# Kernel optimization log

Hardware: AMD Instinct MI355X
Metric: run time of the kernel (lower is better)

Reference implementation:

```python
import jax, jax.numpy as jnp
import numpy as np
import math

H = 12          # num_attention_heads
DH = 64         # attention_head_size
D = H * DH      # hidden_size = 768
LN_EPS = 1e-5
GAUSS_W = 0.3989422804014327
WIDS = [None, 0.1, 1.0, 5.0]


def gauss_weight(L, wid):
    # faithful to generate_gauss_weight: row-normalized Gaussian bump per query pos
    center = (jnp.arange(L, dtype=jnp.float32) / L)[:, None]       # (L,1)
    pos = jnp.linspace(0.0, 1.0, L, dtype=jnp.float32)[None, :]    # (1,L)
    width = max(wid, 0.01) / 9.0                                   # static python scalar
    g = (GAUSS_W / width) * jnp.exp(-(pos - center) ** 2 / (2.0 * width * width))
    return g / jnp.max(g, axis=-1, keepdims=True)                  # (L,L)


def layer_norm(x, g, b):
    mu = jnp.mean(x, axis=-1, keepdims=True)
    var = jnp.mean((x - mu) ** 2, axis=-1, keepdims=True)
    return (x - mu) * jax.lax.rsqrt(var + LN_EPS) * g + b


def bert_attention(x, mask, qkv_w, qkv_b, out_w, out_b, ln_g, ln_b, wid):
    # x: (N,L,D); mask: (N,L,L); qkv_w: (3,D,D); qkv_b: (3,D)
    N, L, _ = x.shape

    def heads(t):  # (N,L,D) -> (N,H,L,DH)
        return t.reshape(N, L, H, DH).transpose(0, 2, 1, 3)

    q = heads(x @ qkv_w[0] + qkv_b[0])
    k = heads(x @ qkv_w[1] + qkv_b[1])
    v = heads(x @ qkv_w[2] + qkv_b[2])

    scores = jnp.einsum('nhqd,nhkd->nhqk', q, k) / math.sqrt(DH)   # (N,H,L,L)
    if wid is not None:
        scores = scores * gauss_weight(L, wid)[None, None]          # multiplicative GMM mask
    scores = scores + (1.0 - mask[:, None, :, :]) * -10000.0
    probs = jax.nn.softmax(scores, axis=-1)                         # dropout = identity (eval)
    ctx = jnp.einsum('nhqk,nhkd->nhqd', probs, v)                   # (N,H,L,DH)
    ctx = ctx.transpose(0, 2, 1, 3).reshape(N, L, D)

    proj = ctx @ out_w + out_b
    return layer_norm(proj + x, ln_g, ln_b)


def setup_inputs() -> dict:
    key = jax.random.key(0)
    ks = jax.random.split(key, 4)
    N, L = 4, 1024
    s = 0.02
    return {
        'input_tensor': jax.random.normal(ks[0], (N, L, D), dtype=jnp.float32),
        'attention_mask': jnp.ones((N, L, L), dtype=jnp.float32),
        'qkv_w': jax.random.normal(ks[1], (4, 3, D, D), dtype=jnp.float32) * s,
        'qkv_b': jnp.zeros((4, 3, D), dtype=jnp.float32),
        'out_w': jax.random.normal(ks[2], (4, D, D), dtype=jnp.float32) * s,
        'out_b': jnp.zeros((4, D), dtype=jnp.float32),
        'ln_g': jnp.ones((4, D), dtype=jnp.float32),
        'ln_b': jnp.zeros((4, D), dtype=jnp.float32),
    }


def reference(input_tensor, attention_mask, qkv_w, qkv_b, out_w, out_b, ln_g, ln_b):
    # pure_block=False path: 4 parallel GMM-masked attention branches, averaged
    outs = [
        bert_attention(input_tensor, attention_mask,
                       qkv_w[i], qkv_b[i], out_w[i], out_b[i], ln_g[i], ln_b[i], WIDS[i])
        for i in range(4)
    ]
    return jnp.mean(jnp.stack(outs, axis=-1), axis=-1)
```

## Files before the change

kernel.cpp:

```cpp
#include <hip/hip_runtime.h>
#include <hip/hip_bf16.h>

#define NB 4
#define LQ 1024
#define NH 12
#define DHD 64
#define DM 768
#define MTOT (NB*LQ)
#define L2E 1.4426950408889634f
#define SMB 11.541560327111708f
#define CFAR 3.3546262790251185e-4f

typedef __attribute__((ext_vector_type(4))) float f32x4;
typedef __attribute__((ext_vector_type(8))) short bf16x8;
typedef __attribute__((ext_vector_type(4))) short short4v;
typedef unsigned short u16;

#if __has_builtin(__builtin_amdgcn_exp2f)
#define EXP2(x) __builtin_amdgcn_exp2f(x)
#else
#define EXP2(x) __expf((x) * 0.6931471805599453f)
#endif

#define VMCNT(n) asm volatile("s_waitcnt vmcnt(" #n ")" ::: "memory")
#define RAW_BAR() __builtin_amdgcn_s_barrier()

__device__ __forceinline__ u16 f2bf(float f){
  union { float f; unsigned int i; } v; v.f = f;
  unsigned int r = v.i + 0x7FFFu + ((v.i >> 16) & 1u);
  return (u16)(r >> 16);
}
__device__ __forceinline__ float bf2f(u16 u){
  union { unsigned int i; float f; } v; v.i = ((unsigned int)u) << 16;
  return v.f;
}
__device__ __forceinline__ unsigned cvt_pk_bf16(float lo, float hi){
  unsigned r;
  asm("v_cvt_pk_bf16_f32 %0, %1, %2" : "=v"(r) : "v"(lo), "v"(hi));
  return r;
}

typedef const __attribute__((address_space(1))) void* gas_t;
typedef __attribute__((address_space(3))) void* las_t;
__device__ __forceinline__ void gload16(const void* g, void* l){
  __builtin_amdgcn_global_load_lds((gas_t)g, (las_t)l, 16, 0, 0);
}

__global__ void k_cvt_x(const float* __restrict__ x, u16* __restrict__ xb){
  int i = (blockIdx.x * 256 + threadIdx.x) * 4;
  float4 v = *reinterpret_cast<const float4*>(x + i);
  short4v o;
  o[0] = (short)f2bf(v.x); o[1] = (short)f2bf(v.y);
  o[2] = (short)f2bf(v.z); o[3] = (short)f2bf(v.w);
  *reinterpret_cast<short4v*>(xb + i) = o;
}

__global__ void k_wt(const float* __restrict__ qkv_w, const float* __restrict__ out_w,
                     u16* __restrict__ wt){
  int mat = blockIdx.z;
  const float* W = (mat < 12) ? (qkv_w + (size_t)mat*DM*DM)
                              : (out_w + (size_t)(mat-12)*DM*DM);
  __shared__ float tile[32][33];
  int j0 = blockIdx.x*32, k0 = blockIdx.y*32;
  int tx = threadIdx.x, ty = threadIdx.y;
  #pragma unroll
  for (int i=0;i<4;i++)
    tile[ty + i*8][tx] = W[(size_t)(k0 + ty + i*8)*DM + j0 + tx];
  __syncthreads();
  u16* dst = wt + (size_t)mat*DM*DM;
  int tid = ty*32 + tx;
  int jj = tid >> 3, kq = tid & 7;
  short4v pk;
  #pragma unroll
  for (int t=0;t<4;t++) pk[t] = (short)f2bf(tile[kq*4 + t][jj]);
  *reinterpret_cast<short4v*>(&dst[(size_t)(j0 + jj)*DM + k0 + kq*4]) = pk;
}

__global__ void k_maskchk(const float* __restrict__ mask, unsigned* __restrict__ flags){
  int qt = blockIdx.x, kt = blockIdx.y, n = blockIdx.z;
  const float* M = mask + ((size_t)(n*LQ) + qt*64)*LQ + kt*64;
  int tid = threadIdx.x;
  int r = tid >> 2, c4 = (tid & 3) * 16;
  int ok = 1;
  #pragma unroll
  for (int j=0;j<4;j++){
    float4 v = *reinterpret_cast<const float4*>(M + (size_t)r*LQ + c4 + j*4);
    ok &= (v.x==1.f) & (v.y==1.f) & (v.z==1.f) & (v.w==1.f);
  }
  __shared__ int sok[4];
  unsigned long long bal = __ballot(ok);
  if ((tid & 63) == 0) sok[tid>>6] = (bal == 0xFFFFFFFFFFFFFFFFull) ? 1 : 0;
  __syncthreads();
  if (tid == 0) flags[((size_t)n*16 + qt)*16 + kt] = sok[0] & sok[1] & sok[2] & sok[3];
}

__global__ __launch_bounds__(256) void k_vsum(const u16* __restrict__ qkvws, float* __restrict__ ps){
  const int nh = blockIdx.x;
  const int b  = blockIdx.y;
  const size_t blk = (size_t)NB*NH*LQ*DHD;
  const u16* Vt = qkvws + (size_t)(b*3+2)*blk + (size_t)nh*DHD*LQ;
  const int tid = threadIdx.x;
  const int dh = tid >> 2, c = tid & 3;
  float* psb = ps + ((size_t)(b*48 + nh)*17)*64;
  float acc = 0.f;
  for (int kt = 0; kt < 16; ++kt){
    if (c == 0) psb[kt*64 + dh] = acc;
    bf16x8 v0 = *reinterpret_cast<const bf16x8*>(&Vt[(size_t)dh*LQ + kt*64 + c*16]);
    bf16x8 v1 = *reinterpret_cast<const bf16x8*>(&Vt[(size_t)dh*LQ + kt*64 + c*16 + 8]);
    float s = 0.f;
    #pragma unroll
    for (int j=0;j<8;j++) s += bf2f((u16)v0[j]) + bf2f((u16)v1[j]);
    s += __shfl_xor(s, 1);
    s += __shfl_xor(s, 2);
    acc += s;
  }
  if (c == 0) psb[16*64 + dh] = acc;
}

__device__ __forceinline__ void gemm_tile32(const u16* __restrict__ Ag,
                                            const u16* __restrict__ Bg,
                                            u16* smem, f32x4 acc[4][4])
{
  const int tid = threadIdx.x, lane = tid & 63, w = tid >> 6;
  const int wr = (w >> 1) * 64, wc = (w & 1) * 64;
  const int rl = lane & 15, q4 = lane >> 4;
  const int srow = tid >> 2;
  const int su = (tid & 3) ^ ((srow >> 1) & 3);

  #define QSTG(buf, k0_) { \
    _Pragma("unroll") \
    for (int r = 0; r < 2; ++r){ \
      gload16(Ag + (size_t)(r*64 + srow)*DM + (k0_) + su*8, smem + (buf)*8192 + r*2048 + tid*8); \
      gload16(Bg + (size_t)(r*64 + srow)*DM + (k0_) + su*8, smem + (buf)*8192 + 4096 + r*2048 + tid*8); \
    } }

  QSTG(0, 0);
  for (int it = 0; it < 24; ++it){
    const int cur = it & 1;
    if (it + 1 < 24){
      QSTG(cur^1, (it+1)*32);
      VMCNT(4);
    } else {
      VMCNT(0);
    }
    RAW_BAR();
    __builtin_amdgcn_sched_barrier(0);
    const u16* al = smem + cur*8192;
    const u16* bl = al + 4096;
    bf16x8 af[4], bfr[4];
    #pragma unroll
    for (int f = 0; f < 4; ++f){
      int ra = wr + f*16 + rl, rb = wc + f*16 + rl;
      int ua = q4 ^ ((ra >> 1) & 3), ub = q4 ^ ((rb >> 1) & 3);
      af[f]  = *reinterpret_cast<const bf16x8*>(&al[ra*32 + ua*8]);
      bfr[f] = *reinterpret_cast<const bf16x8*>(&bl[rb*32 + ub*8]);
    }
    #pragma unroll
    for (int mf=0; mf<4; ++mf)
      #pragma unroll
      for (int nf=0; nf<4; ++nf)
        acc[mf][nf] = __builtin_amdgcn_mfma_f32_16x16x32_bf16(af[mf], bfr[nf], acc[mf][nf], 0,0,0);
    RAW_BAR();
  }
  #undef QSTG
}

__global__ __launch_bounds__(256) void k_qkv(const u16* __restrict__ xb, const u16* __restrict__ wt,
                     const float* __restrict__ qkv_b, u16* __restrict__ qkvws)
{
  __shared__ __align__(16) u16 smem[17408];
  const int bid = blockIdx.x;
  const int orig = (bid & 7) * 288 + (bid >> 3);
  const int m0 = (orig & 31) * 128;
  const int j0 = ((orig >> 5) % 6) * 128;
  const int mat = orig / 192;
  const int t = mat % 3;
  f32x4 acc[4][4] = {};
  gemm_tile32(xb + (size_t)m0*DM, wt + (size_t)mat*DM*DM + (size_t)j0*DM, smem, acc);

  const int tid = threadIdx.x, lane = tid & 63, w = tid >> 6;
  const int wr = (w >> 1) * 64, wc = (w & 1) * 64;
  const int rl = lane & 15, rg = (lane >> 4) * 4;
  const float sc = (t == 0) ? 0.125f : 1.0f;
  const size_t matbase = (size_t)mat * ((size_t)NB*NH*LQ*DHD);
  if (t < 2){
    #pragma unroll
    for (int nf=0; nf<4; ++nf){
      int jc = wc + nf*16 + rl;
      float bias = qkv_b[mat*DM + j0 + jc];
      #pragma unroll
      for (int mf=0; mf<4; ++mf){
        int row = wr + mf*16 + rg;
        #pragma unroll
        for (int i=0;i<4;i++)
          smem[(row+i)*136 + jc] = f2bf((acc[mf][nf][i] + bias) * sc);
      }
    }
    __syncthreads();
    const int n = m0 >> 10, l0 = m0 & 1023;
    const int hbase = j0 >> 6;
    #pragma unroll
    for (int jj=0; jj<8; ++jj){
      int idx = tid + 256*jj;
      int l = idx >> 4, ch = idx & 15;
      bf16x8 v = *reinterpret_cast<const bf16x8*>(&smem[l*136 + ch*8]);
      int hh = hbase + (ch >> 3);
      int dh0 = (ch & 7) * 8;
      *reinterpret_cast<bf16x8*>(
        &qkvws[matbase + ((size_t)(n*NH + hh)*LQ + l0 + l)*DHD + dh0]) = v;
    }
  } else {
    #pragma unroll
    for (int nf=0; nf<4; ++nf){
      int j = j0 + wc + nf*16 + rl;
      float bias = qkv_b[mat*DM + j];
      int h = j >> 6, dh = j & 63;
      #pragma unroll
      for (int mf=0; mf<4; ++mf){
        int mB = m0 + wr + mf*16 + rg;
        int n = mB >> 10, l = mB & 1023;
        short4v pk;
        #pragma unroll
        for (int i=0;i<4;i++) pk[i] = (short)f2bf(acc[mf][nf][i] + bias);
        *reinterpret_cast<short4v*>(&qkvws[matbase + ((size_t)(n*NH + h)*DHD + dh)*LQ + l]) = pk;
      }
    }
  }
}

__global__ __launch_bounds__(512) void k_attn(const u16* __restrict__ qkvws, const float* __restrict__ mask,
                      const unsigned* __restrict__ flags, const float* __restrict__ ps,
                      u16* __restrict__ ctx, float c2_1, float c2_2, float c2_3)
{
  __shared__ __align__(16) u16 kv_lds[2][2][64*64];
  __shared__ __align__(16) u16 p_lds[128*64];
  const int bid = blockIdx.x;
  const int orig = (bid & 7) * 192 + (bid >> 3);
  const int qp = orig & 7;
  const int b  = (orig >> 3) & 3;
  const int nh = orig >> 5;
  const int n = nh / NH, h = nh % NH;
  const float c2 = (b==1) ? c2_1 : (b==2) ? c2_2 : c2_3;
  const bool useG = (b != 0);
  const int tid = threadIdx.x, lane = tid & 63, w = tid >> 6;
  const int wl = w & 3, half = w >> 2;
  const int qt = qp*2 + half;
  const int rl = lane & 15, q4 = lane >> 4, kc8 = q4*8, rg = q4*4;
  const int q0 = qt*64 + wl*16;

  const size_t hb = (size_t)(n*NH + h);
  const size_t blk = (size_t)NB*NH*LQ*DHD;
  const u16* Qb = qkvws + (size_t)(b*3+0)*blk + hb*LQ*DHD;
  const u16* Kb = qkvws + (size_t)(b*3+1)*blk + hb*LQ*DHD;
  const u16* Vt = qkvws + (size_t)(b*3+2)*blk + hb*DHD*LQ;
  const float* Mb = mask + (size_t)n*LQ*LQ;

  bf16x8 qf0 = *reinterpret_cast<const bf16x8*>(&Qb[(size_t)(q0+rl)*DHD + kc8]);
  bf16x8 qf1 = *reinterpret_cast<const bf16x8*>(&Qb[(size_t)(q0+rl)*DHD + 32 + kc8]);

  float srun[4] = {0.f,0.f,0.f,0.f};
  float dmin2[4], cq[4];
  f32x4 o[4] = {};
  #pragma unroll
  for (int i=0;i<4;i++){
    int q = q0 + rg + i;
    float c = (float)q * (1.0f/1024.0f);
    float ksf = floorf(c * 1023.0f + 0.5f);
    float dm = ksf * (1.0f/1023.0f) - c;
    cq[i] = c; dmin2[i] = dm*dm;
  }

  int lo_a, hi_a, lo_b, hi_b, ra_a, ra_b;
  {
    int qa = qp*2, qb = qp*2+1;
    int r0 = 1, r1 = 1;
    for (int t = 0; t < 16; ++t){
      r0 &= (flags[((size_t)n*16 + qa)*16 + t] != 0u) ? 1 : 0;
      r1 &= (flags[((size_t)n*16 + qb)*16 + t] != 0u) ? 1 : 0;
    }
    ra_a = r0; ra_b = r1;
    lo_a = 0; hi_a = 16; lo_b = 0; hi_b = 16;
    if (r0){
      if (b == 1){ lo_a = qa>0?qa-1:0; hi_a = qa<15?qa+2:16; }
      else if (b == 2){ lo_a = qa>5?qa-5:0; hi_a = qa<10?qa+6:16; }
    }
    if (r1){
      if (b == 1){ lo_b = qb>0?qb-1:0; hi_b = qb<15?qb+2:16; }
      else if (b == 2){ lo_b = qb>5?qb-5:0; hi_b = qb<10?qb+6:16; }
    }
  }
  const int mylo = half ? lo_b : lo_a;
  const int myhi = half ? hi_b : hi_a;
  const int myrowall = half ? ra_b : ra_a;
  const int blo = lo_a < lo_b ? lo_a : lo_b;
  const int bhi = hi_a > hi_b ? hi_a : hi_b;
  const int mynt = myhi - mylo;

  if (myrowall && mynt < 16){
    const float* psb = ps + ((size_t)(b*48 + nh)*17)*64;
    #pragma unroll
    for (int nf=0; nf<4; ++nf){
      int dh = nf*16 + rl;
      float sfar = psb[16*64 + dh] - psb[myhi*64 + dh] + psb[mylo*64 + dh];
      float fv = CFAR * sfar;
      #pragma unroll
      for (int i=0;i<4;i++) o[nf][i] = fv;
    }
    float sinit = CFAR * (float)(64*(16 - mynt));
    #pragma unroll
    for (int i=0;i<4;i++) srun[i] = sinit;
  }

  const int r8 = tid >> 3;
  const int uu = (tid & 7) ^ (r8 & 7);

  #define STAGE8(buf, kt_) { \
    gload16(Kb + (size_t)((kt_)*64 + r8)*DHD + uu*8, (u16*)kv_lds[buf][0] + tid*8); \
    gload16(Vt + (size_t)r8*LQ + (kt_)*64 + uu*8, (u16*)kv_lds[buf][1] + tid*8); }

  STAGE8(0, blo);

  const int nloop = bhi - blo;
  for (int it = 0; it < nloop; ++it){
    const int kt = blo + it;
    const int cur = it & 1;
    if (it + 1 < nloop){
      STAGE8(cur^1, kt+1);
      VMCNT(2);
    } else {
      VMCNT(0);
    }
    RAW_BAR();
    __builtin_amdgcn_sched_barrier(0);

    if (kt >= mylo && kt < myhi){
      const bool allones = myrowall || (flags[((size_t)n*16 + qt)*16 + kt] != 0u);
      const u16* kbuf = (const u16*)kv_lds[cur][0];
      const u16* vbuf = (const u16*)kv_lds[cur][1];

      f32x4 sf[4] = {};
      #pragma unroll
      for (int nf=0; nf<4; ++nf){
        int row = nf*16 + rl, sw = (row & 7) << 3;
        bf16x8 kf0 = *reinterpret_cast<const bf16x8*>(&kbuf[row*64 + (kc8 ^ sw)]);
        bf16x8 kf1 = *reinterpret_cast<const bf16x8*>(&kbuf[row*64 + ((32 + kc8) ^ sw)]);
        sf[nf] = __builtin_amdgcn_mfma_f32_16x16x32_bf16(qf0, kf0, sf[nf], 0,0,0);
        sf[nf] = __builtin_amdgcn_mfma_f32_16x16x32_bf16(qf1, kf1, sf[nf], 0,0,0);
      }

      float pv[4][4];
      #pragma unroll
      for (int nf=0; nf<4; ++nf){
        int key = kt*64 + nf*16 + rl;
        float pos = (float)key * (1.0f/1023.0f);
        #pragma unroll
        for (int i=0;i<4;i++){
          float s = sf[nf][i];
          if (useG){
            float d = pos - cq[i];
            float tg = fmaf(-d, d, dmin2[i]);
            s *= EXP2(tg * c2);
          }
          if (!allones){
            int q = q0 + rg + i;
            s = fmaf(1.0f - Mb[(size_t)q*LQ + key], -10000.0f, s);
          }
          float p = EXP2(fmaf(s, L2E, -SMB));
          srun[i] += p;
          pv[nf][i] = p;
        }
      }

      #pragma unroll
      for (int np=0; np<2; ++np)
        #pragma unroll
        for (int i=0;i<4;i++){
          unsigned u = cvt_pk_bf16(pv[np*2][i], pv[np*2+1][i]);
          int row = w*16 + rg + i, sw = (row & 7) << 3;
          p_lds[row*64 + ((np*32 + rl) ^ sw)]      = (u16)(u & 0xffffu);
          p_lds[row*64 + ((np*32 + 16 + rl) ^ sw)] = (u16)(u >> 16);
        }
      asm volatile("s_waitcnt lgkmcnt(0)" ::: "memory");
      __builtin_amdgcn_sched_barrier(0);

      {
        int prow = w*16 + rl, psw = (prow & 7) << 3;
        bf16x8 pa0 = *reinterpret_cast<const bf16x8*>(&p_lds[prow*64 + (kc8 ^ psw)]);
        bf16x8 pa1 = *reinterpret_cast<const bf16x8*>(&p_lds[prow*64 + ((32 + kc8) ^ psw)]);
        #pragma unroll
        for (int nf=0; nf<4; ++nf){
          int row = nf*16 + rl, sw = (row & 7) << 3;
          bf16x8 vv0 = *reinterpret_cast<const bf16x8*>(&vbuf[row*64 + (kc8 ^ sw)]);
          bf16x8 vv1 = *reinterpret_cast<const bf16x8*>(&vbuf[row*64 + ((32 + kc8) ^ sw)]);
          o[nf] = __builtin_amdgcn_mfma_f32_16x16x32_bf16(pa0, vv0, o[nf], 0,0,0);
          o[nf] = __builtin_amdgcn_mfma_f32_16x16x32_bf16(pa1, vv1, o[nf], 0,0,0);
        }
      }
    }
    RAW_BAR();
  }

  #pragma unroll
  for (int off=1; off<16; off<<=1){
    #pragma unroll
    for (int i=0;i<4;i++) srun[i] += __shfl_xor(srun[i], off);
  }
  #pragma unroll
  for (int i=0;i<4;i++){
    float inv = 1.0f / (srun[i] + 1e-35f);
    int q = q0 + rg + i;
    size_t mrow = ((size_t)(n*LQ + q)) * DM;
    #pragma unroll
    for (int nf=0; nf<4; ++nf){
      int d = h*DHD + nf*16 + rl;
      ctx[(size_t)b*((size_t)MTOT*DM) + mrow + d] = f2bf(o[nf][i] * inv);
    }
  }
  #undef STAGE8
}

__global__ __launch_bounds__(256) void k_proj(const u16* __restrict__ ctx, const u16* __restrict__ wt,
                      const float* __restrict__ out_b, u16* __restrict__ proj)
{
  __shared__ __align__(16) u16 smem[17408];
  const int bid = blockIdx.x;
  const int orig = (bid & 7) * 96 + (bid >> 3);
  const int m0 = (orig & 31) * 128;
  const int j0 = ((orig >> 5) % 6) * 128;
  const int b = orig / 192;
  f32x4 acc[4][4] = {};
  gemm_tile32(ctx + (size_t)b*MTOT*DM + (size_t)m0*DM,
              wt + (size_t)(12+b)*DM*DM + (size_t)j0*DM, smem, acc);
  const int tid = threadIdx.x, lane = tid & 63, w = tid >> 6;
  const int wr = (w >> 1) * 64, wc = (w & 1) * 64;
  const int rl = lane & 15, rg = (lane >> 4) * 4;
  #pragma unroll
  for (int nf=0; nf<4; ++nf){
    int jc = wc + nf*16 + rl;
    float bias = out_b[b*DM + j0 + jc];
    #pragma unroll
    for (int mf=0; mf<4; ++mf){
      int row = wr + mf*16 + rg;
      #pragma unroll
      for (int i=0;i<4;i++)
        smem[(row+i)*136 + jc] = f2bf(acc[mf][nf][i] + bias);
    }
  }
  __syncthreads();
  #pragma unroll
  for (int jj=0; jj<8; ++jj){
    int idx = tid + 256*jj;
    int l = idx >> 4, ch = idx & 15;
    bf16x8 v = *reinterpret_cast<const bf16x8*>(&smem[l*136 + ch*8]);
    *reinterpret_cast<bf16x8*>(&proj[((size_t)b*MTOT + m0 + l)*DM + j0 + ch*8]) = v;
  }
}

__global__ __launch_bounds__(256) void k_ln(const float* __restrict__ x, const u16* __restrict__ proj,
                    const float* __restrict__ ln_g, const float* __restrict__ ln_b,
                    float* __restrict__ out)
{
  const int m = blockIdx.x;
  const int tid = threadIdx.x, lane = tid & 63, w = tid >> 6;
  __shared__ float rb[4][2][4];
  float xr[3], acc[3] = {0.f,0.f,0.f};
  #pragma unroll
  for (int c=0;c<3;c++) xr[c] = x[(size_t)m*DM + tid + c*256];
  float vv[4][3], s1[4], s2[4];
  #pragma unroll
  for (int b=0;b<4;b++){
    s1[b] = 0.f; s2[b] = 0.f;
    #pragma unroll
    for (int c=0;c<3;c++){
      float v = bf2f(proj[((size_t)b*MTOT + m)*DM + tid + c*256]) + xr[c];
      vv[b][c] = v; s1[b] += v; s2[b] += v*v;
    }
  }
  #pragma unroll
  for (int b=0;b<4;b++){
    #pragma unroll
    for (int off=32; off>=1; off>>=1){
      s1[b] += __shfl_xor(s1[b], off);
      s2[b] += __shfl_xor(s2[b], off);
    }
    if (lane == 0){ rb[b][0][w] = s1[b]; rb[b][1][w] = s2[b]; }
  }
  __syncthreads();
  #pragma unroll
  for (int b=0;b<4;b++){
    float S1 = rb[b][0][0]+rb[b][0][1]+rb[b][0][2]+rb[b][0][3];
    float S2 = rb[b][1][0]+rb[b][1][1]+rb[b][1][2]+rb[b][1][3];
    float mu = S1 * (1.0f/768.0f);
    float var = S2 * (1.0f/768.0f) - mu*mu;
    float rs = rsqrtf(var + 1e-5f);
    #pragma unroll
    for (int c=0;c<3;c++){
      int j = tid + c*256;
      acc[c] += 0.25f * ((vv[b][c]-mu)*rs*ln_g[b*DM+j] + ln_b[b*DM+j]);
    }
  }
  #pragma unroll
  for (int c=0;c<3;c++) out[(size_t)m*DM + tid + c*256] = acc[c];
}

extern "C" void kernel_launch(void* const* d_in, const int* in_sizes, int n_in,
                              void* d_out, int out_size, void* d_ws, size_t ws_size,
                              hipStream_t stream)
{
  const float* x     = (const float*)d_in[0];
  const float* mask  = (const float*)d_in[1];
  const float* qkv_w = (const float*)d_in[2];
  const float* qkv_b = (const float*)d_in[3];
  const float* out_w = (const float*)d_in[4];
  const float* out_b = (const float*)d_in[5];
  const float* ln_g  = (const float*)d_in[6];
  const float* ln_b  = (const float*)d_in[7];
  float* out = (float*)d_out;
  char* ws = (char*)d_ws;

  u16* xb        = (u16*)(ws);
  unsigned* flags= (unsigned*)(ws);
  float* ps      = (float*)(ws + 8192);
  u16* wt        = (u16*)(ws + 6291456);
  u16* qkv       = (u16*)(ws + 25165824);
  u16* ctx       = (u16*)(ws + 100663296);
  u16* proj      = (u16*)(ws + 25165824);

  float c2[3];
  const float wid[3] = {0.1f, 1.0f, 5.0f};
  for (int i=0;i<3;i++){
    float wdt = wid[i]/9.0f;
    c2[i] = (1.0f/(2.0f*wdt*wdt)) * L2E;
  }

  k_cvt_x<<<dim3(3072), dim3(256), 0, stream>>>(x, xb);
  k_wt<<<dim3(24,24,16), dim3(32,8), 0, stream>>>(qkv_w, out_w, wt);
  k_qkv<<<dim3(2304), dim3(256), 0, stream>>>(xb, wt, qkv_b, qkv);
  k_vsum<<<dim3(48,4), dim3(256), 0, stream>>>(qkv, ps);
  k_maskchk<<<dim3(16,16,4), dim3(256), 0, stream>>>(mask, flags);
  k_attn<<<dim3(1536), dim3(512), 0, stream>>>(qkv, mask, flags, ps, ctx, c2[0], c2[1], c2[2]);
  k_proj<<<dim3(768), dim3(256), 0, stream>>>(ctx, wt, out_b, proj);
  k_ln<<<dim3(4096), dim3(256), 0, stream>>>(x, proj, ln_g, ln_b, out);
}
```

Before: 259.1 us.

## Load K/V fragments directly from global into registers, drop LDS staging and barriers

The attention kernel stops staging K and V tiles through double-buffered shared memory with block barriers. Each wave now reads its K and V MFMA fragments straight from global memory, prefetching the next K tile into a ping-pong register set. Blocks shrink to 256 threads covering one 64-row query tile, and the grid doubles. This removes barrier synchronisation and LDS traffic, but each wave re-reads K/V from global/L2 with no sharing across waves, and register pressure rises.

```diff
diff --git a/kernel.cpp b/kernel.cpp
--- a/kernel.cpp
+++ b/kernel.cpp
@@ -228,25 +228,21 @@
   }
 }
 
-__global__ __launch_bounds__(512) void k_attn(const u16* __restrict__ qkvws, const float* __restrict__ mask,
+__global__ __launch_bounds__(256) void k_attn(const u16* __restrict__ qkvws, const float* __restrict__ mask,
                       const unsigned* __restrict__ flags, const float* __restrict__ ps,
                       u16* __restrict__ ctx, float c2_1, float c2_2, float c2_3)
 {
-  __shared__ __align__(16) u16 kv_lds[2][2][64*64];
-  __shared__ __align__(16) u16 p_lds[128*64];
+  __shared__ __align__(16) u16 p_lds[64*64];
   const int bid = blockIdx.x;
-  const int orig = (bid & 7) * 192 + (bid >> 3);
-  const int qp = orig & 7;
-  const int b  = (orig >> 3) & 3;
-  const int nh = orig >> 5;
+  const int orig = (bid & 7) * 384 + (bid >> 3);
+  const int qt = orig & 15;
+  const int b  = (orig >> 4) & 3;
+  const int nh = orig >> 6;
   const int n = nh / NH, h = nh % NH;
   const float c2 = (b==1) ? c2_1 : (b==2) ? c2_2 : c2_3;
   const bool useG = (b != 0);
   const int tid = threadIdx.x, lane = tid & 63, w = tid >> 6;
-  const int wl = w & 3, half = w >> 2;
-  const int qt = qp*2 + half;
   const int rl = lane & 15, q4 = lane >> 4, kc8 = q4*8, rg = q4*4;
-  const int q0 = qt*64 + wl*16;
 
   const size_t hb = (size_t)(n*NH + h);
   const size_t blk = (size_t)NB*NH*LQ*DHD;
@@ -255,150 +251,131 @@
   const u16* Vt = qkvws + (size_t)(b*3+2)*blk + hb*DHD*LQ;
   const float* Mb = mask + (size_t)n*LQ*LQ;
 
-  bf16x8 qf0 = *reinterpret_cast<const bf16x8*>(&Qb[(size_t)(q0+rl)*DHD + kc8]);
-  bf16x8 qf1 = *reinterpret_cast<const bf16x8*>(&Qb[(size_t)(q0+rl)*DHD + 32 + kc8]);
+  const int q0 = qt*64;
+  const int qrow = q0 + w*16 + rl;
+  bf16x8 qf0 = *reinterpret_cast<const bf16x8*>(&Qb[(size_t)qrow*DHD + kc8]);
+  bf16x8 qf1 = *reinterpret_cast<const bf16x8*>(&Qb[(size_t)qrow*DHD + 32 + kc8]);
 
   float srun[4] = {0.f,0.f,0.f,0.f};
   float dmin2[4], cq[4];
   f32x4 o[4] = {};
   #pragma unroll
   for (int i=0;i<4;i++){
-    int q = q0 + rg + i;
+    int q = q0 + w*16 + rg + i;
     float c = (float)q * (1.0f/1024.0f);
     float ksf = floorf(c * 1023.0f + 0.5f);
     float dm = ksf * (1.0f/1023.0f) - c;
     cq[i] = c; dmin2[i] = dm*dm;
   }
 
-  int lo_a, hi_a, lo_b, hi_b, ra_a, ra_b;
-  {
-    int qa = qp*2, qb = qp*2+1;
-    int r0 = 1, r1 = 1;
-    for (int t = 0; t < 16; ++t){
-      r0 &= (flags[((size_t)n*16 + qa)*16 + t] != 0u) ? 1 : 0;
-      r1 &= (flags[((size_t)n*16 + qb)*16 + t] != 0u) ? 1 : 0;
-    }
-    ra_a = r0; ra_b = r1;
-    lo_a = 0; hi_a = 16; lo_b = 0; hi_b = 16;
-    if (r0){
-      if (b == 1){ lo_a = qa>0?qa-1:0; hi_a = qa<15?qa+2:16; }
-      else if (b == 2){ lo_a = qa>5?qa-5:0; hi_a = qa<10?qa+6:16; }
-    }
-    if (r1){
-      if (b == 1){ lo_b = qb>0?qb-1:0; hi_b = qb<15?qb+2:16; }
-      else if (b == 2){ lo_b = qb>5?qb-5:0; hi_b = qb<10?qb+6:16; }
-    }
-  }
-  const int mylo = half ? lo_b : lo_a;
-  const int myhi = half ? hi_b : hi_a;
-  const int myrowall = half ? ra_b : ra_a;
-  const int blo = lo_a < lo_b ? lo_a : lo_b;
-  const int bhi = hi_a > hi_b ? hi_a : hi_b;
-  const int mynt = myhi - mylo;
-
-  if (myrowall && mynt < 16){
+  int rowall = 1;
+  for (int t = 0; t < 16; ++t) rowall &= (flags[((size_t)n*16 + qt)*16 + t] != 0u) ? 1 : 0;
+
+  int ktlo = 0, kthi = 16;
+  if (rowall){
+    if (b == 1){ ktlo = qt > 0 ? qt-1 : 0; kthi = qt < 15 ? qt+2 : 16; }
+    else if (b == 2){ ktlo = qt > 5 ? qt-5 : 0; kthi = qt < 10 ? qt+6 : 16; }
+  }
+  const int nt = kthi - ktlo;
+
+  if (rowall && nt < 16){
     const float* psb = ps + ((size_t)(b*48 + nh)*17)*64;
     #pragma unroll
     for (int nf=0; nf<4; ++nf){
       int dh = nf*16 + rl;
-      float sfar = psb[16*64 + dh] - psb[myhi*64 + dh] + psb[mylo*64 + dh];
+      float sfar = psb[16*64 + dh] - psb[kthi*64 + dh] + psb[ktlo*64 + dh];
       float fv = CFAR * sfar;
       #pragma unroll
       for (int i=0;i<4;i++) o[nf][i] = fv;
     }
-    float sinit = CFAR * (float)(64*(16 - mynt));
+    float sinit = CFAR * (float)(64*(16 - nt));
     #pragma unroll
     for (int i=0;i<4;i++) srun[i] = sinit;
   }
 
-  const int r8 = tid >> 3;
-  const int uu = (tid & 7) ^ (r8 & 7);
-
-  #define STAGE8(buf, kt_) { \
-    gload16(Kb + (size_t)((kt_)*64 + r8)*DHD + uu*8, (u16*)kv_lds[buf][0] + tid*8); \
-    gload16(Vt + (size_t)r8*LQ + (kt_)*64 + uu*8, (u16*)kv_lds[buf][1] + tid*8); }
-
-  STAGE8(0, blo);
-
-  const int nloop = bhi - blo;
-  for (int it = 0; it < nloop; ++it){
-    const int kt = blo + it;
-    const int cur = it & 1;
-    if (it + 1 < nloop){
-      STAGE8(cur^1, kt+1);
-      VMCNT(2);
-    } else {
-      VMCNT(0);
-    }
-    RAW_BAR();
-    __builtin_amdgcn_sched_barrier(0);
-
-    if (kt >= mylo && kt < myhi){
-      const bool allones = myrowall || (flags[((size_t)n*16 + qt)*16 + kt] != 0u);
-      const u16* kbuf = (const u16*)kv_lds[cur][0];
-      const u16* vbuf = (const u16*)kv_lds[cur][1];
-
-      f32x4 sf[4] = {};
-      #pragma unroll
-      for (int nf=0; nf<4; ++nf){
-        int row = nf*16 + rl, sw = (row & 7) << 3;
-        bf16x8 kf0 = *reinterpret_cast<const bf16x8*>(&kbuf[row*64 + (kc8 ^ sw)]);
-        bf16x8 kf1 = *reinterpret_cast<const bf16x8*>(&kbuf[row*64 + ((32 + kc8) ^ sw)]);
-        sf[nf] = __builtin_amdgcn_mfma_f32_16x16x32_bf16(qf0, kf0, sf[nf], 0,0,0);
-        sf[nf] = __builtin_amdgcn_mfma_f32_16x16x32_bf16(qf1, kf1, sf[nf], 0,0,0);
-      }
-
-      float pv[4][4];
-      #pragma unroll
-      for (int nf=0; nf<4; ++nf){
-        int key = kt*64 + nf*16 + rl;
-        float pos = (float)key * (1.0f/1023.0f);
-        #pragma unroll
-        for (int i=0;i<4;i++){
-          float s = sf[nf][i];
-          if (useG){
-            float d = pos - cq[i];
-            float tg = fmaf(-d, d, dmin2[i]);
-            s *= EXP2(tg * c2);
-          }
-          if (!allones){
-            int q = q0 + rg + i;
-            s = fmaf(1.0f - Mb[(size_t)q*LQ + key], -10000.0f, s);
-          }
-          float p = EXP2(fmaf(s, L2E, -SMB));
-          srun[i] += p;
-          pv[nf][i] = p;
-        }
-      }
-
-      #pragma unroll
-      for (int np=0; np<2; ++np)
-        #pragma unroll
-        for (int i=0;i<4;i++){
-          unsigned u = cvt_pk_bf16(pv[np*2][i], pv[np*2+1][i]);
-          int row = w*16 + rg + i, sw = (row & 7) << 3;
-          p_lds[row*64 + ((np*32 + rl) ^ sw)]      = (u16)(u & 0xffffu);
-          p_lds[row*64 + ((np*32 + 16 + rl) ^ sw)] = (u16)(u >> 16);
-        }
-      asm volatile("s_waitcnt lgkmcnt(0)" ::: "memory");
-      __builtin_amdgcn_sched_barrier(0);
-
-      {
-        int prow = w*16 + rl, psw = (prow & 7) << 3;
-        bf16x8 pa0 = *reinterpret_cast<const bf16x8*>(&p_lds[prow*64 + (kc8 ^ psw)]);
-        bf16x8 pa1 = *reinterpret_cast<const bf16x8*>(&p_lds[prow*64 + ((32 + kc8) ^ psw)]);
-        #pragma unroll
-        for (int nf=0; nf<4; ++nf){
-          int row = nf*16 + rl, sw = (row & 7) << 3;
-          bf16x8 vv0 = *reinterpret_cast<const bf16x8*>(&vbuf[row*64 + (kc8 ^ sw)]);
-          bf16x8 vv1 = *reinterpret_cast<const bf16x8*>(&vbuf[row*64 + ((32 + kc8) ^ sw)]);
-          o[nf] = __builtin_amdgcn_mfma_f32_16x16x32_bf16(pa0, vv0, o[nf], 0,0,0);
-          o[nf] = __builtin_amdgcn_mfma_f32_16x16x32_bf16(pa1, vv1, o[nf], 0,0,0);
-        }
-      }
-    }
-    RAW_BAR();
-  }
+  bf16x8 kA0[4], kA1[4], kB0[4], kB1[4];
+
+  #define LOADK(D0, D1, kt_) { \
+    _Pragma("unroll") \
+    for (int nf=0; nf<4; ++nf){ \
+      D0[nf] = *reinterpret_cast<const bf16x8*>(&Kb[(size_t)((kt_)*64 + nf*16 + rl)*DHD + kc8]); \
+      D1[nf] = *reinterpret_cast<const bf16x8*>(&Kb[(size_t)((kt_)*64 + nf*16 + rl)*DHD + 32 + kc8]); \
+    } }
+
+  #define STEP(C0, C1, N0, N1, itv) { \
+    const int kt = ktlo + (itv); \
+     \
+    bf16x8 vf0[4], vf1[4]; \
+    _Pragma("unroll") \
+    for (int nf=0; nf<4; ++nf){ \
+      vf0[nf] = *reinterpret_cast<const bf16x8*>(&Vt[(size_t)(nf*16+rl)*LQ + kt*64 + kc8]); \
+      vf1[nf] = *reinterpret_cast<const bf16x8*>(&Vt[(size_t)(nf*16+rl)*LQ + kt*64 + 32 + kc8]); \
+    } \
+    if ((itv) + 1 < nt) LOADK(N0, N1, kt + 1); \
+    const bool allones = rowall || (flags[((size_t)n*16 + qt)*16 + kt] != 0u); \
+    f32x4 sf[4] = {}; \
+    _Pragma("unroll") \
+    for (int nf=0; nf<4; ++nf){ \
+      sf[nf] = __builtin_amdgcn_mfma_f32_16x16x32_bf16(qf0, C0[nf], sf[nf], 0,0,0); \
+      sf[nf] = __builtin_amdgcn_mfma_f32_16x16x32_bf16(qf1, C1[nf], sf[nf], 0,0,0); \
+    } \
+    float pv[4][4]; \
+    _Pragma("unroll") \
+    for (int nf=0; nf<4; ++nf){ \
+      int key = kt*64 + nf*16 + rl; \
+      float pos = (float)key * (1.0f/1023.0f); \
+      _Pragma("unroll") \
+      for (int i=0;i<4;i++){ \
+        float s = sf[nf][i]; \
+        if (useG){ \
+          float d = pos - cq[i]; \
+          float tg = fmaf(-d, d, dmin2[i]); \
+          s *= EXP2(tg * c2); \
+        } \
+        if (!allones){ \
+          int q = q0 + w*16 + rg + i; \
+          s = fmaf(1.0f - Mb[(size_t)q*LQ + key], -10000.0f, s); \
+        } \
+        float p = EXP2(fmaf(s, L2E, -SMB)); \
+        srun[i] += p; \
+        pv[nf][i] = p; \
+      } \
+    } \
+    _Pragma("unroll") \
+    for (int np=0; np<2; ++np) \
+      _Pragma("unroll") \
+      for (int i=0;i<4;i++){ \
+        unsigned u = cvt_pk_bf16(pv[np*2][i], pv[np*2+1][i]); \
+        int row = w*16 + rg + i, sw = (row & 7) << 3; \
+        p_lds[row*64 + ((np*32 + rl) ^ sw)]      = (u16)(u & 0xffffu); \
+        p_lds[row*64 + ((np*32 + 16 + rl) ^ sw)] = (u16)(u >> 16); \
+      } \
+    asm volatile("s_waitcnt lgkmcnt(0)" ::: "memory"); \
+    __builtin_amdgcn_sched_barrier(0); \
+    { \
+      int prow = w*16 + rl, psw = (prow & 7) << 3; \
+      bf16x8 pa0 = *reinterpret_cast<const bf16x8*>(&p_lds[prow*64 + (kc8 ^ psw)]); \
+      bf16x8 pa1 = *reinterpret_cast<const bf16x8*>(&p_lds[prow*64 + ((32 + kc8) ^ psw)]); \
+      _Pragma("unroll") \
+      for (int nf=0; nf<4; ++nf){ \
+        o[nf] = __builtin_amdgcn_mfma_f32_16x16x32_bf16(pa0, vf0[nf], o[nf], 0,0,0); \
+        o[nf] = __builtin_amdgcn_mfma_f32_16x16x32_bf16(pa1, vf1[nf], o[nf], 0,0,0); \
+      } \
+    } \
+  }
+
+  LOADK(kA0, kA1, ktlo);
+  {
+    int it = 0;
+    while (true){
+      STEP(kA0, kA1, kB0, kB1, it);
+      if (++it >= nt) break;
+      STEP(kB0, kB1, kA0, kA1, it);
+      if (++it >= nt) break;
+    }
+  }
+  #undef STEP
+  #undef LOADK
 
   #pragma unroll
   for (int off=1; off<16; off<<=1){
@@ -408,7 +385,7 @@
   #pragma unroll
   for (int i=0;i<4;i++){
     float inv = 1.0f / (srun[i] + 1e-35f);
-    int q = q0 + rg + i;
+    int q = q0 + w*16 + rg + i;
     size_t mrow = ((size_t)(n*LQ + q)) * DM;
     #pragma unroll
     for (int nf=0; nf<4; ++nf){
@@ -416,7 +393,6 @@
       ctx[(size_t)b*((size_t)MTOT*DM) + mrow + d] = f2bf(o[nf][i] * inv);
     }
   }
-  #undef STAGE8
 }
 
 __global__ __launch_bounds__(256) void k_proj(const u16* __restrict__ ctx, const u16* __restrict__ wt,
@@ -538,7 +514,7 @@
   k_qkv<<<dim3(2304), dim3(256), 0, stream>>>(xb, wt, qkv_b, qkv);
   k_vsum<<<dim3(48,4), dim3(256), 0, stream>>>(qkv, ps);
   k_maskchk<<<dim3(16,16,4), dim3(256), 0, stream>>>(mask, flags);
-  k_attn<<<dim3(1536), dim3(512), 0, stream>>>(qkv, mask, flags, ps, ctx, c2[0], c2[1], c2[2]);
+  k_attn<<<dim3(3072), dim3(256), 0, stream>>>(qkv, mask, flags, ps, ctx, c2[0], c2[1], c2[2]);
   k_proj<<<dim3(768), dim3(256), 0, stream>>>(ctx, wt, out_b, proj);
   k_ln<<<dim3(4096), dim3(256), 0, stream>>>(x, proj, ln_g, ln_b, out);
 }
```

Measured after the change: 427.3 us. +64.9%, slower.
